# Optimization experiments

Measured on AMD Instinct MI355X. Metric: run time of the kernel, lower is better.

## Reference

```python
import jax, jax.numpy as jnp
import numpy as np

B, T, N_EMBED, HEADSIZE = 16, 2048, 1024, 128


def setup_inputs() -> dict:
    key = jax.random.key(0)
    kx, kq, kk, kv = jax.random.split(key, 4)
    x = jax.random.normal(kx, (B, T, N_EMBED), dtype=jnp.float32)
    # nn.Linear(n_embed, headsize, bias=False): y = x @ W, W stored [n_embed, headsize]
    s = (1.0 / np.sqrt(N_EMBED)).astype(np.float32)
    Wq = jax.random.normal(kq, (N_EMBED, HEADSIZE), dtype=jnp.float32) * s
    Wk = jax.random.normal(kk, (N_EMBED, HEADSIZE), dtype=jnp.float32) * s
    Wv = jax.random.normal(kv, (N_EMBED, HEADSIZE), dtype=jnp.float32) * s
    return {"x": x, "Wq": Wq, "Wk": Wk, "Wv": Wv}


def reference(x, Wq, Wk, Wv):
    Bsz, Tlen, C = x.shape
    q = x @ Wq  # [B, T, H]
    k = x @ Wk  # [B, T, H]
    v = x @ Wv  # [B, T, H]
    scale = C ** (-0.5)  # NOTE: original scales by n_embed**-0.5, not headsize**-0.5
    wt = jnp.einsum('bqh,bkh->bqk', q, k) * scale  # [B, T, T]
    causal = jnp.tril(jnp.ones((Tlen, Tlen), dtype=bool))
    wt = jnp.where(causal, wt, -jnp.inf)
    wt = jax.nn.softmax(wt, axis=-1)
    # dropout is identity in eval mode
    out = jnp.einsum('bqk,bkh->bqh', wt, v)  # [B, T, H]
    return out
```

## Files before the change

### kernel.cpp

```cpp
#include <hip/hip_runtime.h>
#include <hip/hip_bf16.h>

#define BATCH 16
#define TLEN 2048
#define CDIM 1024
#define HDIM 128

typedef __attribute__((ext_vector_type(8))) short bf16x8;
typedef __attribute__((ext_vector_type(4))) float f32x4;
typedef __attribute__((ext_vector_type(16))) float f32x16;
typedef __attribute__((ext_vector_type(4))) unsigned short u16x4;
typedef __attribute__((ext_vector_type(8))) unsigned short u16x8;

static __device__ __forceinline__ unsigned short f2bf(float f) {
    __hip_bfloat16 h = __float2bfloat16(f);
    return *(unsigned short*)&h;
}
static __device__ __forceinline__ unsigned pkbf(float a, float b) {
    return (unsigned)f2bf(a) | ((unsigned)f2bf(b) << 16);
}
static __device__ __forceinline__ int part_offs(int qc) {
    return qc + ((qc * qc - 2 * qc + (qc & 1)) >> 2);
}

typedef const __attribute__((address_space(1))) unsigned int* gas_t;
typedef __attribute__((address_space(3))) unsigned int* las_t;
static __device__ __forceinline__ void gl_lds16(const void* g, void* l) {
    __builtin_amdgcn_global_load_lds((gas_t)g, (las_t)l, 16, 0, 0);
}

static __device__ __forceinline__ void hard_barrier() {
    __builtin_amdgcn_sched_barrier(0);
    __builtin_amdgcn_s_barrier();
    __builtin_amdgcn_sched_barrier(0);
}

__global__ __launch_bounds__(256) void pack_w(
    const float* __restrict__ Wq, const float* __restrict__ Wk,
    const float* __restrict__ Wv, unsigned short* __restrict__ wtb)
{
    const int which = blockIdx.y;
    const float* W = (which == 0) ? Wq : (which == 1) ? Wk : Wv;
    const int n = blockIdx.x >> 2;
    const int k = (blockIdx.x & 3) * 256 + threadIdx.x;
    wtb[((size_t)which * 128 + n) * 1024 + k] = f2bf(W[(size_t)k * 128 + n]);
}

__global__ __launch_bounds__(256, 2) void qkv_fused(
    const float* __restrict__ x, const unsigned short* __restrict__ wtb,
    unsigned short* __restrict__ qb, unsigned short* __restrict__ kb,
    unsigned short* __restrict__ vtb)
{
    __shared__ __align__(16) float          Axf[2][64 * 64];
    __shared__ __align__(16) unsigned short Bs[2][192 * 64];

    const int xcd = blockIdx.x & 7, s = blockIdx.x >> 3;
    const int m0 = (xcd * 64 + (s >> 1)) * 64;
    const int nh = s & 1;

    const int tid  = threadIdx.x;
    const int lane = tid & 63, wid = tid >> 6;
    const int c = lane & 15, g = lane >> 4;

    f32x4 acc[4][3];
#pragma unroll
    for (int i = 0; i < 4; ++i)
#pragma unroll
        for (int j = 0; j < 3; ++j) acc[i][j] = (f32x4){0.f, 0.f, 0.f, 0.f};

#define STAGE(k0_, bi_)                                                      \
    { _Pragma("unroll")                                                      \
      for (int i_ = 0; i_ < 4; ++i_) {                                       \
          const int seg_ = wid * 4 + i_;                                     \
          const int row_ = seg_ * 4 + (lane >> 4);                           \
          const int sg_  = (lane & 15) ^ (row_ & 15);                        \
          gl_lds16(x + (size_t)(m0 + row_) * CDIM + (k0_) + sg_ * 4,         \
                   (char*)Axf[bi_] + seg_ * 1024);                           \
      }                                                                      \
      _Pragma("unroll")                                                      \
      for (int i_ = 0; i_ < 6; ++i_) {                                       \
          const int seg_ = wid * 6 + i_;                                     \
          const int row_ = seg_ * 8 + (lane >> 3);                           \
          const int sg_  = (lane & 7) ^ (row_ & 7);                          \
          gl_lds16(wtb + (size_t)(nh * 192 + row_) * 1024 + (k0_) + sg_ * 8, \
                   (char*)Bs[bi_] + seg_ * 1024);                            \
      } }

    STAGE(0, 0);

#pragma unroll 1
    for (int kt = 0; kt < 16; ++kt) {
        const int bi = kt & 1;
        if (kt < 15) {
            STAGE((kt + 1) * 64, bi ^ 1);
            asm volatile("s_waitcnt vmcnt(10)" ::: "memory");
        } else {
            asm volatile("s_waitcnt vmcnt(0)" ::: "memory");
        }
        hard_barrier();

#pragma unroll
        for (int ks = 0; ks < 2; ++ks) {
            bf16x8 af[4], bf[3];
#pragma unroll
            for (int mf = 0; mf < 4; ++mf) {
                const int rm = mf * 16 + c;
                const float* base = Axf[bi] + rm * 64;
                const int g0 = (ks * 8 + 2 * g)     ^ (rm & 15);
                const int g1 = (ks * 8 + 2 * g + 1) ^ (rm & 15);
                f32x4 lo = *(const f32x4*)(base + g0 * 4);
                f32x4 hi = *(const f32x4*)(base + g1 * 4);
                bf16x8 t;
                t[0] = f2bf(lo[0]); t[1] = f2bf(lo[1]); t[2] = f2bf(lo[2]); t[3] = f2bf(lo[3]);
                t[4] = f2bf(hi[0]); t[5] = f2bf(hi[1]); t[6] = f2bf(hi[2]); t[7] = f2bf(hi[3]);
                af[mf] = t;
            }
#pragma unroll
            for (int nf = 0; nf < 3; ++nf) {
                const int rn = wid * 48 + nf * 16 + c;
                const int gb = (ks * 4 + g) ^ (rn & 7);
                bf[nf] = *(const bf16x8*)((char*)Bs[bi] + rn * 128 + gb * 16);
            }

            __builtin_amdgcn_s_setprio(1);
#pragma unroll
            for (int mf = 0; mf < 4; ++mf)
#pragma unroll
                for (int nf = 0; nf < 3; ++nf)
                    acc[mf][nf] = __builtin_amdgcn_mfma_f32_16x16x32_bf16(
                        af[mf], bf[nf], acc[mf][nf], 0, 0, 0);
            __builtin_amdgcn_s_setprio(0);
        }

        hard_barrier();
    }

#pragma unroll
    for (int mf = 0; mf < 4; ++mf) {
#pragma unroll
        for (int nf = 0; nf < 3; ++nf) {
            const int col0 = nh * 192 + wid * 48 + nf * 16;
            const int nt = col0 >> 7;
            const int nc = (col0 & 127) + c;
            const int m = m0 + mf * 16 + g * 4;
            if (nt == 0) {
#pragma unroll
                for (int r = 0; r < 4; ++r)
                    qb[(size_t)(m + r) * HDIM + nc] = f2bf(acc[mf][nf][r] * 0.03125f);
            } else if (nt == 1) {
#pragma unroll
                for (int r = 0; r < 4; ++r)
                    kb[(size_t)(m + r) * HDIM + nc] = f2bf(acc[mf][nf][r]);
            } else {
                const int b = m >> 11, tl = m & (TLEN - 1);
                u16x4 o;
                o[0] = f2bf(acc[mf][nf][0]); o[1] = f2bf(acc[mf][nf][1]);
                o[2] = f2bf(acc[mf][nf][2]); o[3] = f2bf(acc[mf][nf][3]);
                *(u16x4*)(vtb + ((size_t)b * HDIM + nc) * TLEN + tl) = o;
            }
        }
    }
#undef STAGE
}

__global__ __launch_bounds__(256, 2) void attn_partial(
    const short* __restrict__ qb, const short* __restrict__ kb,
    const short* __restrict__ vtb,
    unsigned short* __restrict__ Opart, float* __restrict__ mpart,
    float* __restrict__ lpart)
{
    const int kc = blockIdx.x;
    const int qc = blockIdx.y;
    const int b  = blockIdx.z;
    if (kc > (qc >> 1)) return;
    const int kv_base = kc * 256;
    const int qrel = qc * 128 - kv_base;
    int NT = ((qrel + 127) >> 6) + 1; if (NT > 4) NT = 4;

    __shared__ unsigned short Ks[2][64 * 128];
    __shared__ unsigned short Vs[2][128 * 64];

    const int tid  = threadIdx.x;
    const int wid  = tid >> 6;
    const int lane = tid & 63;
    const int c5 = lane & 31, hi = lane >> 5;
    const int q0w = qc * 128 + wid * 32;
    const int qg  = q0w + c5;
    const int pidx = b * 72 + part_offs(qc) + kc;

    const short* Kb  = kb  + (size_t)b * TLEN * HDIM;
    const short* Vtb = vtb + (size_t)b * HDIM * TLEN;

    bf16x8 qf[8];
#pragma unroll
    for (int ks = 0; ks < 8; ++ks)
        qf[ks] = *(const bf16x8*)(qb + ((size_t)b * TLEN + qg) * HDIM + ks * 16 + hi * 8);

    bf16x8 kst[4], vst[4];

#define GLOAD(kv0_)                                                          \
    {                                                                        \
        _Pragma("unroll")                                                    \
        for (int it = 0; it < 4; ++it) {                                     \
            const int o = tid * 16 + it * 4096;                              \
            const int kr = o >> 8, kcb = o & 0xF0;                           \
            kst[it] = *(const bf16x8*)((const char*)Kb +                     \
                        (size_t)((kv0_) + kr) * 256 + kcb);                  \
            const int vr = o >> 7, vcb = o & 0x70;                           \
            vst[it] = *(const bf16x8*)((const char*)Vtb +                    \
                        (size_t)vr * (TLEN * 2) + (size_t)(kv0_) * 2 + vcb); \
        }                                                                    \
    }
#define SSTORE(bi_)                                                          \
    {                                                                        \
        _Pragma("unroll")                                                    \
        for (int it = 0; it < 4; ++it) {                                     \
            const int o = tid * 16 + it * 4096;                              \
            const int kr = o >> 8, kcb = o & 0xF0;                           \
            *(bf16x8*)((char*)Ks[bi_] + kr * 256 + (kcb ^ ((kr & 7) << 4))) = kst[it]; \
            const int vr = o >> 7, vcb = o & 0x70;                           \
            *(bf16x8*)((char*)Vs[bi_] + vr * 128 + (vcb ^ ((vr & 7) << 4))) = vst[it]; \
        }                                                                    \
    }

    GLOAD(kv_base);
    SSTORE(0);
    __syncthreads();

    f32x16 oacc[4];
#pragma unroll
    for (int i = 0; i < 4; ++i)
#pragma unroll
        for (int r = 0; r < 16; ++r) oacc[i][r] = 0.f;
    float m_r = -1e30f;
    float l_r = 0.f;

#pragma unroll 1
    for (int t = 0; t < NT; ++t) {
        const int bi = t & 1;
        if (t + 1 < NT) GLOAD(kv_base + 64 * (t + 1));

        const int kv0 = kv_base + 64 * t;
        if (kv0 <= q0w + 31) {
            f32x16 s0, s1;
#pragma unroll
            for (int r = 0; r < 16; ++r) { s0[r] = 0.f; s1[r] = 0.f; }
            __builtin_amdgcn_s_setprio(1);
#pragma unroll
            for (int ks = 0; ks < 8; ++ks) {
                const int col = ks * 32 + hi * 16;
                const int off0 = c5 * 256 + (col ^ ((c5 & 7) << 4));
                const int off1 = (32 + c5) * 256 + (col ^ ((c5 & 7) << 4));
                bf16x8 a0 = *(const bf16x8*)((char*)Ks[bi] + off0);
                bf16x8 a1 = *(const bf16x8*)((char*)Ks[bi] + off1);
                s0 = __builtin_amdgcn_mfma_f32_32x32x16_bf16(a0, qf[ks], s0, 0, 0, 0);
                s1 = __builtin_amdgcn_mfma_f32_32x32x16_bf16(a1, qf[ks], s1, 0, 0, 0);
            }
            __builtin_amdgcn_s_setprio(0);

            if (kv0 + 63 > q0w) {
#pragma unroll
                for (int r = 0; r < 16; ++r) {
                    const int key0 = kv0 + (r & 3) + 8 * (r >> 2) + 4 * hi;
                    if (key0 > qg)      s0[r] = -INFINITY;
                    if (key0 + 32 > qg) s1[r] = -INFINITY;
                }
            }

            float t8[8];
#pragma unroll
            for (int i = 0; i < 8; ++i)
                t8[i] = fmaxf(fmaxf(s0[2*i], s0[2*i+1]), fmaxf(s1[2*i], s1[2*i+1]));
            float smax = fmaxf(fmaxf(fmaxf(t8[0], t8[1]), fmaxf(t8[2], t8[3])),
                               fmaxf(fmaxf(t8[4], t8[5]), fmaxf(t8[6], t8[7])));
            smax = fmaxf(smax, __shfl_xor(smax, 32));

            const bool defer = __all(smax - m_r <= 8.0f);
            const float mnew = defer ? m_r : fmaxf(m_r, smax);
            if (!defer) {
                const float alpha = __expf(m_r - mnew);
                l_r *= alpha;
#pragma unroll
                for (int hb = 0; hb < 4; ++hb) oacc[hb] = oacc[hb] * alpha;
            }
            m_r = mnew;

#pragma unroll
            for (int r = 0; r < 16; ++r) {
                s0[r] = __expf(s0[r] - mnew);
                s1[r] = __expf(s1[r] - mnew);
            }
            float a8[8];
#pragma unroll
            for (int i = 0; i < 8; ++i)
                a8[i] = (s0[2*i] + s0[2*i+1]) + (s1[2*i] + s1[2*i+1]);
            float psum = ((a8[0] + a8[1]) + (a8[2] + a8[3])) +
                         ((a8[4] + a8[5]) + (a8[6] + a8[7]));
            psum += __shfl_xor(psum, 32);
            l_r += psum;

            bf16x8 pa[4];
#pragma unroll
            for (int kb2 = 0; kb2 < 2; ++kb2) {
#pragma unroll
                for (int par = 0; par < 2; ++par) {
                    const int e = par * 8;
                    float v0, v1, v2, v3, v4, v5, v6, v7;
                    if (kb2 == 0) {
                        v0=s0[e+0]; v1=s0[e+1]; v2=s0[e+2]; v3=s0[e+3];
                        v4=s0[e+4]; v5=s0[e+5]; v6=s0[e+6]; v7=s0[e+7];
                    } else {
                        v0=s1[e+0]; v1=s1[e+1]; v2=s1[e+2]; v3=s1[e+3];
                        v4=s1[e+4]; v5=s1[e+5]; v6=s1[e+6]; v7=s1[e+7];
                    }
                    const unsigned w0 = pkbf(v0, v1), w1 = pkbf(v2, v3);
                    const unsigned w2 = pkbf(v4, v5), w3 = pkbf(v6, v7);
                    const unsigned X0 = hi ? w0 : w2;
                    const unsigned X1 = hi ? w1 : w3;
                    const unsigned R0 = (unsigned)__shfl_xor((int)X0, 32);
                    const unsigned R1 = (unsigned)__shfl_xor((int)X1, 32);
                    union { unsigned w[4]; bf16x8 v; } uu;
                    uu.w[0] = hi ? R0 : w0;  uu.w[1] = hi ? R1 : w1;
                    uu.w[2] = hi ? w2 : R0;  uu.w[3] = hi ? w3 : R1;
                    pa[kb2 * 2 + par] = uu.v;
                }
            }

            __builtin_amdgcn_s_setprio(1);
#pragma unroll
            for (int hb = 0; hb < 4; ++hb) {
                const int row = hb * 32 + c5;
#pragma unroll
                for (int ks = 0; ks < 4; ++ks) {
                    const int off = row * 128 + ((ks * 32 + hi * 16) ^ ((row & 7) << 4));
                    bf16x8 va = *(const bf16x8*)((char*)Vs[bi] + off);
                    oacc[hb] = __builtin_amdgcn_mfma_f32_32x32x16_bf16(va, pa[ks], oacc[hb], 0, 0, 0);
                }
            }
            __builtin_amdgcn_s_setprio(0);
        }

        if (t + 1 < NT) {
            SSTORE(bi ^ 1);
            __syncthreads();
        }
    }

    __syncthreads();
    char* sl = (char*)Ks + wid * 8192;
#pragma unroll
    for (int hb = 0; hb < 4; ++hb)
#pragma unroll
        for (int rq = 0; rq < 4; ++rq) {
            u16x4 o4;
            o4[0] = f2bf(oacc[hb][rq * 4 + 0]);
            o4[1] = f2bf(oacc[hb][rq * 4 + 1]);
            o4[2] = f2bf(oacc[hb][rq * 4 + 2]);
            o4[3] = f2bf(oacc[hb][rq * 4 + 3]);
            const int off = c5 * 256 + ((hb * 64 + rq * 16 + hi * 8) ^ ((c5 & 7) << 4));
            *(u16x4*)(sl + off) = o4;
        }
    asm volatile("s_waitcnt lgkmcnt(0)" ::: "memory");
    __builtin_amdgcn_sched_barrier(0);

    const int qr = lane >> 1, hf = lane & 1;
    unsigned short* Og = Opart + (size_t)pidx * 128 * 128 +
                         (size_t)(wid * 32 + qr) * 128 + hf * 64;
#pragma unroll
    for (int i = 0; i < 8; ++i) {
        const int off = qr * 256 + ((hf * 128 + i * 16) ^ ((qr & 7) << 4));
        *(u16x8*)(Og + i * 8) = *(const u16x8*)(sl + off);
    }
    if (hi == 0) {
        mpart[(size_t)pidx * 128 + wid * 32 + c5] = m_r;
        lpart[(size_t)pidx * 128 + wid * 32 + c5] = l_r;
    }
#undef GLOAD
#undef SSTORE
}

__global__ __launch_bounds__(256) void attn_combine(
    const unsigned short* __restrict__ Opart, const float* __restrict__ mpart,
    const float* __restrict__ lpart, float* __restrict__ out)
{
    const int qc = blockIdx.x;
    const int b  = blockIdx.y;
    const int n  = (qc >> 1) + 1;
    const int base = b * 72 + part_offs(qc);
    const int t   = threadIdx.x;
    const int row = t >> 1;
    const int d0  = (t & 1) * 64;

    float M = -INFINITY;
    for (int p = 0; p < n; ++p)
        M = fmaxf(M, mpart[(size_t)(base + p) * 128 + row]);
    float L = 0.f;
    for (int p = 0; p < n; ++p)
        L += __expf(mpart[(size_t)(base + p) * 128 + row] - M) *
             lpart[(size_t)(base + p) * 128 + row];

    float acc[64];
#pragma unroll
    for (int i = 0; i < 64; ++i) acc[i] = 0.f;

    for (int p = 0; p < n; ++p) {
        const float w = __expf(mpart[(size_t)(base + p) * 128 + row] - M);
        const bf16x8* src = (const bf16x8*)(Opart +
            ((size_t)(base + p) * 128 + row) * 128 + d0);
#pragma unroll
        for (int j = 0; j < 8; ++j) {
            bf16x8 v = src[j];
#pragma unroll
            for (int e = 0; e < 8; ++e) {
                union { unsigned u; float f; } x;
                x.u = ((unsigned)(unsigned short)v[e]) << 16;
                acc[j * 8 + e] += w * x.f;
            }
        }
    }

    const float invL = 1.f / L;
    float4* dst = (float4*)(out + ((size_t)(b * TLEN + qc * 128 + row)) * 128 + d0);
#pragma unroll
    for (int i = 0; i < 16; ++i)
        dst[i] = make_float4(acc[4*i] * invL, acc[4*i+1] * invL,
                             acc[4*i+2] * invL, acc[4*i+3] * invL);
}

extern "C" void kernel_launch(void* const* d_in, const int* in_sizes, int n_in,
                              void* d_out, int out_size, void* d_ws, size_t ws_size,
                              hipStream_t stream)
{
    const float* x  = (const float*)d_in[0];
    const float* Wq = (const float*)d_in[1];
    const float* Wk = (const float*)d_in[2];
    const float* Wv = (const float*)d_in[3];
    float* outp = (float*)d_out;

    const size_t per = (size_t)BATCH * TLEN * HDIM;
    unsigned short* qb  = (unsigned short*)d_ws;
    unsigned short* kb  = qb + per;
    unsigned short* vtb = kb + per;
    unsigned short* wtb = vtb + per;
    unsigned short* Opart = wtb + 384 * 1024;
    float* mpart = (float*)(Opart + (size_t)1152 * 128 * 128);
    float* lpart = mpart + (size_t)1152 * 128;

    dim3 gw(512, 3);
    pack_w<<<gw, 256, 0, stream>>>(Wq, Wk, Wv, wtb);

    qkv_fused<<<1024, 256, 0, stream>>>(x, wtb, qb, kb, vtb);

    dim3 g2(8, 16, BATCH);
    attn_partial<<<g2, 256, 0, stream>>>((const short*)qb, (const short*)kb,
                                         (const short*)vtb, Opart, mpart, lpart);

    dim3 g3(16, BATCH);
    attn_combine<<<g3, 256, 0, stream>>>(Opart, mpart, lpart, outp);
}
```

Before: 136.7 us.

## Convert x to bf16 once per tile in registers and enlarge QKV GEMM tile

The QKV projection kernel now loads x tiles into registers, converts them to bf16 once, and writes bf16 into LDS. Previously fp32 was staged in LDS and every wave reconverted it on each fragment read. The tile grows to 128x192 with 512 threads (2x4 waves), which halves the number of blocks and reuses the weight tile across twice as many rows. The cost is register-staged A loads that need a wait before the LDS write, plus a different occupancy point (launch bounds 512,4).

New measurement: 130.0 us. 4.9% less time.

```diff
diff --git a/kernel.cpp b/kernel.cpp
--- a/kernel.cpp
+++ b/kernel.cpp
@@ -46,82 +46,89 @@
     wtb[((size_t)which * 128 + n) * 1024 + k] = f2bf(W[(size_t)k * 128 + n]);
 }
 
-__global__ __launch_bounds__(256, 2) void qkv_fused(
+__global__ __launch_bounds__(512, 4) void qkv_fused(
     const float* __restrict__ x, const unsigned short* __restrict__ wtb,
     unsigned short* __restrict__ qb, unsigned short* __restrict__ kb,
     unsigned short* __restrict__ vtb)
 {
-    __shared__ __align__(16) float          Axf[2][64 * 64];
-    __shared__ __align__(16) unsigned short Bs[2][192 * 64];
+    __shared__ __align__(16) unsigned short Ab[2][128 * 64];
+    __shared__ __align__(16) unsigned short Bb[2][192 * 64];
 
     const int xcd = blockIdx.x & 7, s = blockIdx.x >> 3;
-    const int m0 = (xcd * 64 + (s >> 1)) * 64;
+    const int m0 = (xcd * 32 + (s >> 1)) * 128;
     const int nh = s & 1;
 
     const int tid  = threadIdx.x;
     const int lane = tid & 63, wid = tid >> 6;
+    const int wm = wid >> 2, wn = wid & 3;
     const int c = lane & 15, g = lane >> 4;
 
+    const int arow = tid >> 2, aq = tid & 3;
+    const float* xsrc = x + (size_t)(m0 + arow) * CDIM + aq * 16;
+
     f32x4 acc[4][3];
 #pragma unroll
     for (int i = 0; i < 4; ++i)
 #pragma unroll
         for (int j = 0; j < 3; ++j) acc[i][j] = (f32x4){0.f, 0.f, 0.f, 0.f};
 
-#define STAGE(k0_, bi_)                                                      \
+    float4 As0, As1, As2, As3;
+
+#define AISSUE(k0_)                                                          \
+    { const float* s_ = xsrc + (k0_);                                        \
+      As0 = *(const float4*)(s_);      As1 = *(const float4*)(s_ + 4);       \
+      As2 = *(const float4*)(s_ + 8);  As3 = *(const float4*)(s_ + 12); }
+
+#define AWRITE(bi_)                                                          \
+    { u16x8 t0_, t1_;                                                        \
+      t0_[0]=f2bf(As0.x); t0_[1]=f2bf(As0.y); t0_[2]=f2bf(As0.z); t0_[3]=f2bf(As0.w); \
+      t0_[4]=f2bf(As1.x); t0_[5]=f2bf(As1.y); t0_[6]=f2bf(As1.z); t0_[7]=f2bf(As1.w); \
+      t1_[0]=f2bf(As2.x); t1_[1]=f2bf(As2.y); t1_[2]=f2bf(As2.z); t1_[3]=f2bf(As2.w); \
+      t1_[4]=f2bf(As3.x); t1_[5]=f2bf(As3.y); t1_[6]=f2bf(As3.z); t1_[7]=f2bf(As3.w); \
+      char* ba_ = (char*)Ab[bi_] + arow * 128;                               \
+      *(u16x8*)(ba_ + ((aq * 32 +  0) ^ ((arow & 7) << 4))) = t0_;           \
+      *(u16x8*)(ba_ + ((aq * 32 + 16) ^ ((arow & 7) << 4))) = t1_; }
+
+#define BISSUE(k0_, bi_)                                                     \
     { _Pragma("unroll")                                                      \
-      for (int i_ = 0; i_ < 4; ++i_) {                                       \
-          const int seg_ = wid * 4 + i_;                                     \
-          const int row_ = seg_ * 4 + (lane >> 4);                           \
-          const int sg_  = (lane & 15) ^ (row_ & 15);                        \
-          gl_lds16(x + (size_t)(m0 + row_) * CDIM + (k0_) + sg_ * 4,         \
-                   (char*)Axf[bi_] + seg_ * 1024);                           \
-      }                                                                      \
-      _Pragma("unroll")                                                      \
-      for (int i_ = 0; i_ < 6; ++i_) {                                       \
-          const int seg_ = wid * 6 + i_;                                     \
+      for (int i_ = 0; i_ < 3; ++i_) {                                       \
+          const int seg_ = wid * 3 + i_;                                     \
           const int row_ = seg_ * 8 + (lane >> 3);                           \
-          const int sg_  = (lane & 7) ^ (row_ & 7);                          \
-          gl_lds16(wtb + (size_t)(nh * 192 + row_) * 1024 + (k0_) + sg_ * 8, \
-                   (char*)Bs[bi_] + seg_ * 1024);                            \
+          const int gr_  = (lane & 7) ^ (row_ & 7);                          \
+          gl_lds16(wtb + (size_t)(nh * 192 + row_) * 1024 + (k0_) + gr_ * 8, \
+                   (char*)Bb[bi_] + seg_ * 1024);                            \
       } }
 
-    STAGE(0, 0);
+    AISSUE(0);
+    BISSUE(0, 0);
+    asm volatile("s_waitcnt vmcnt(3)" ::: "memory");
+    AWRITE(0);
+    asm volatile("s_waitcnt vmcnt(0) lgkmcnt(0)" ::: "memory");
+    hard_barrier();
 
 #pragma unroll 1
     for (int kt = 0; kt < 16; ++kt) {
-        const int bi = kt & 1;
+        const int cur = kt & 1;
         if (kt < 15) {
-            STAGE((kt + 1) * 64, bi ^ 1);
-            asm volatile("s_waitcnt vmcnt(10)" ::: "memory");
-        } else {
-            asm volatile("s_waitcnt vmcnt(0)" ::: "memory");
-        }
-        hard_barrier();
+            AISSUE((kt + 1) * 64);
+            BISSUE((kt + 1) * 64, cur ^ 1);
+        }
 
 #pragma unroll
         for (int ks = 0; ks < 2; ++ks) {
             bf16x8 af[4], bf[3];
 #pragma unroll
             for (int mf = 0; mf < 4; ++mf) {
-                const int rm = mf * 16 + c;
-                const float* base = Axf[bi] + rm * 64;
-                const int g0 = (ks * 8 + 2 * g)     ^ (rm & 15);
-                const int g1 = (ks * 8 + 2 * g + 1) ^ (rm & 15);
-                f32x4 lo = *(const f32x4*)(base + g0 * 4);
-                f32x4 hi = *(const f32x4*)(base + g1 * 4);
-                bf16x8 t;
-                t[0] = f2bf(lo[0]); t[1] = f2bf(lo[1]); t[2] = f2bf(lo[2]); t[3] = f2bf(lo[3]);
-                t[4] = f2bf(hi[0]); t[5] = f2bf(hi[1]); t[6] = f2bf(hi[2]); t[7] = f2bf(hi[3]);
-                af[mf] = t;
+                const int rm = wm * 64 + mf * 16 + c;
+                af[mf] = *(const bf16x8*)((char*)Ab[cur] + rm * 128 +
+                                          ((ks * 64 + g * 16) ^ ((rm & 7) << 4)));
             }
 #pragma unroll
             for (int nf = 0; nf < 3; ++nf) {
-                const int rn = wid * 48 + nf * 16 + c;
-                const int gb = (ks * 4 + g) ^ (rn & 7);
-                bf[nf] = *(const bf16x8*)((char*)Bs[bi] + rn * 128 + gb * 16);
-            }
-
+                const int rn = wn * 48 + nf * 16 + c;
+                bf[nf] = *(const bf16x8*)((char*)Bb[cur] + rn * 128 +
+                                          ((ks * 64 + g * 16) ^ ((rn & 7) << 4)));
+            }
             __builtin_amdgcn_s_setprio(1);
 #pragma unroll
             for (int mf = 0; mf < 4; ++mf)
@@ -132,17 +139,22 @@
             __builtin_amdgcn_s_setprio(0);
         }
 
-        hard_barrier();
+        if (kt < 15) {
+            asm volatile("s_waitcnt vmcnt(3)" ::: "memory");
+            AWRITE(cur ^ 1);
+            asm volatile("s_waitcnt vmcnt(0) lgkmcnt(0)" ::: "memory");
+            hard_barrier();
+        }
     }
 
 #pragma unroll
     for (int mf = 0; mf < 4; ++mf) {
 #pragma unroll
         for (int nf = 0; nf < 3; ++nf) {
-            const int col0 = nh * 192 + wid * 48 + nf * 16;
+            const int col0 = nh * 192 + wn * 48 + nf * 16;
             const int nt = col0 >> 7;
             const int nc = (col0 & 127) + c;
-            const int m = m0 + mf * 16 + g * 4;
+            const int m = m0 + wm * 64 + mf * 16 + g * 4;
             if (nt == 0) {
 #pragma unroll
                 for (int r = 0; r < 4; ++r)
@@ -160,7 +172,9 @@
             }
         }
     }
-#undef STAGE
+#undef AISSUE
+#undef AWRITE
+#undef BISSUE
 }
 
 __global__ __launch_bounds__(256, 2) void attn_partial(
@@ -412,9 +426,9 @@
             bf16x8 v = src[j];
 #pragma unroll
             for (int e = 0; e < 8; ++e) {
-                union { unsigned u; float f; } x;
-                x.u = ((unsigned)(unsigned short)v[e]) << 16;
-                acc[j * 8 + e] += w * x.f;
+                union { unsigned u; float f; } xx;
+                xx.u = ((unsigned)(unsigned short)v[e]) << 16;
+                acc[j * 8 + e] += w * xx.f;
             }
         }
     }
@@ -449,7 +463,7 @@
     dim3 gw(512, 3);
     pack_w<<<gw, 256, 0, stream>>>(Wq, Wk, Wv, wtb);
 
-    qkv_fused<<<1024, 256, 0, stream>>>(x, wtb, qb, kb, vtb);
+    qkv_fused<<<512, 512, 0, stream>>>(x, wtb, qb, kb, vtb);
 
     dim3 g2(8, 16, BATCH);
     attn_partial<<<g2, 256, 0, stream>>>((const short*)qb, (const short*)kb,
```
